# Kernel optimization log

Measured on AMD Instinct MI355X. Metric: run time of the kernel, lower is better.

## Reference

```python
import jax, jax.numpy as jnp
import numpy as np

N_RES = 131072
MSA_C = 384
HID = 128
N_BLOCK = 2
N_RESTYPE = 21


def l2_normalize(x, eps=1e-12):
    s = jnp.sum(x.astype(jnp.float32) ** 2, axis=-1, keepdims=True)
    return (x / jnp.sqrt(jnp.maximum(s, eps))).astype(x.dtype)


def quat_to_rot(q):
    q = q / jnp.sqrt(jnp.maximum(jnp.sum(q * q, axis=-1, keepdims=True), 1e-12))
    w, x, y, z = q[..., 0], q[..., 1], q[..., 2], q[..., 3]
    r00 = 1 - 2 * (y * y + z * z); r01 = 2 * (x * y - w * z); r02 = 2 * (x * z + w * y)
    r10 = 2 * (x * y + w * z); r11 = 1 - 2 * (x * x + z * z); r12 = 2 * (y * z - w * x)
    r20 = 2 * (x * z - w * y); r21 = 2 * (y * z + w * x); r22 = 1 - 2 * (x * x + y * y)
    return jnp.stack([jnp.stack([r00, r01, r02], -1),
                      jnp.stack([r10, r11, r12], -1),
                      jnp.stack([r20, r21, r22], -1)], axis=-2)


def setup_inputs() -> dict:
    key = jax.random.key(0)
    ks = jax.random.split(key, 20)
    d = {}
    d['affine'] = jax.random.normal(ks[0], (N_RES, 7), jnp.float32)
    d['rep0'] = jax.random.normal(ks[1], (N_RES, MSA_C), jnp.float32)
    d['rep1'] = jax.random.normal(ks[2], (N_RES, MSA_C), jnp.float32)
    d['aatype'] = jax.random.randint(ks[3], (N_RES,), 0, N_RESTYPE, jnp.int32)
    sc = 0.05
    d['w_in0'] = jax.random.normal(ks[4], (MSA_C, HID), jnp.float32) * sc
    d['b_in0'] = jnp.zeros((HID,), jnp.float32)
    d['w_in1'] = jax.random.normal(ks[5], (MSA_C, HID), jnp.float32) * sc
    d['b_in1'] = jnp.zeros((HID,), jnp.float32)
    d['Wr1'] = jax.random.normal(ks[6], (N_BLOCK, HID, HID), jnp.float32) * sc
    d['br1'] = jnp.zeros((N_BLOCK, HID), jnp.float32)
    d['Wr2'] = jax.random.normal(ks[7], (N_BLOCK, HID, HID), jnp.float32) * sc
    d['br2'] = jnp.zeros((N_BLOCK, HID), jnp.float32)
    d['w_ang'] = jax.random.normal(ks[8], (HID, 14), jnp.float32) * sc
    d['b_ang'] = jnp.zeros((14,), jnp.float32)
    # literature geometry tables (AF2 shapes; random stand-ins for correctness baseline)
    d['default_frames'] = jax.random.normal(ks[9], (N_RESTYPE, 8, 4, 4), jnp.float32)
    d['group_idx'] = jax.random.randint(ks[10], (N_RESTYPE, 14), 0, 8, jnp.int32)
    d['atom_mask'] = (jax.random.uniform(ks[11], (N_RESTYPE, 14)) > 0.2).astype(jnp.float32)
    d['lit_positions'] = jax.random.normal(ks[12], (N_RESTYPE, 14, 3), jnp.float32)
    return d


def reference(affine, rep0, rep1, aatype, w_in0, b_in0, w_in1, b_in1, Wr1, br1,
              Wr2, br2, w_ang, b_ang, default_frames, group_idx, atom_mask, lit_positions):
    # MLP trunk
    act = (jax.nn.relu(rep0) @ w_in0 + b_in0) + (jax.nn.relu(rep1) @ w_in1 + b_in1)
    for i in range(Wr1.shape[0]):
        old = act
        act = jax.nn.relu(act) @ Wr1[i] + br1[i]
        act = jax.nn.relu(act) @ Wr2[i] + br2[i]
        act = act + old
    n = act.shape[0]
    unnorm = (jax.nn.relu(act) @ w_ang + b_ang).reshape(n, 7, 2)
    angles = l2_normalize(unnorm)

    # backbone rigid from quat-affine
    rot_b = quat_to_rot(affine[:, :4])          # [N,3,3]
    trans_b = affine[:, 4:]                     # [N,3]

    # torsion_angles_to_frames
    sin = jnp.concatenate([jnp.zeros((n, 1), angles.dtype), angles[..., 0]], axis=-1)  # [N,8]
    cos = jnp.concatenate([jnp.ones((n, 1), angles.dtype), angles[..., 1]], axis=-1)
    z = jnp.zeros_like(sin); o = jnp.ones_like(sin)
    all_rots = jnp.stack([jnp.stack([o, z, z], -1),
                          jnp.stack([z, cos, -sin], -1),
                          jnp.stack([z, sin, cos], -1)], axis=-2)     # [N,8,3,3]
    m = default_frames[aatype]                   # [N,8,4,4] gather
    rot_f = jnp.einsum('ngij,ngjk->ngik', m[..., :3, :3], all_rots)   # [N,8,3,3]
    trans_f = m[..., :3, 3]                      # [N,8,3]

    def compose(r1, t1, r2, t2):
        return jnp.einsum('nij,njk->nik', r1, r2), jnp.einsum('nij,nj->ni', r1, t2) + t1

    r5, t5 = compose(rot_f[:, 4], trans_f[:, 4], rot_f[:, 5], trans_f[:, 5])  # chi2->backb
    r6, t6 = compose(r5, t5, rot_f[:, 6], trans_f[:, 6])                       # chi3->backb
    r7, t7 = compose(r6, t6, rot_f[:, 7], trans_f[:, 7])                       # chi4->backb
    rot_all = jnp.concatenate([rot_f[:, :5], jnp.stack([r5, r6, r7], 1)], axis=1)    # [N,8,3,3]
    trans_all = jnp.concatenate([trans_f[:, :5], jnp.stack([t5, t6, t7], 1)], axis=1)

    rot_g = jnp.einsum('nij,ngjk->ngik', rot_b, rot_all)                # [N,8,3,3]
    trans_g = jnp.einsum('nij,ngj->ngi', rot_b, trans_all) + trans_b[:, None]

    # frames_and_literature_positions_to_atom14_pos
    gm = jax.nn.one_hot(group_idx[aatype], 8, dtype=rot_g.dtype)        # [N,14,8]
    rot_a = jnp.einsum('nag,ngij->naij', gm, rot_g)                     # [N,14,3,3]
    trans_a = jnp.einsum('nag,ngi->nai', gm, trans_g)                   # [N,14,3]
    lit = lit_positions[aatype]                                         # [N,14,3]
    pos = jnp.einsum('naij,naj->nai', rot_a, lit) + trans_a
    pos = pos * atom_mask[aatype][..., None]
    return angles, unnorm, pos, rot_g, trans_g
```

## Files before the change

### kernel.cpp

```cpp
#include <hip/hip_runtime.h>
#include <stdint.h>

typedef _Float16 f16x8 __attribute__((ext_vector_type(8)));
typedef float floatx4 __attribute__((ext_vector_type(4)));

__device__ __forceinline__ void f2h2(float x, unsigned short& hi, unsigned short& lo) {
  _Float16 h = (_Float16)x;
  float r = (x - (float)h) * 2048.0f;
  _Float16 l = (_Float16)r;
  union { _Float16 f; unsigned short u; } a, b;
  a.f = h; b.f = l;
  hi = a.u; lo = b.u;
}

__device__ __forceinline__ void async_copy16(void* lds, const void* gsrc) {
  __builtin_amdgcn_global_load_lds(
      (const __attribute__((address_space(1))) unsigned int*)gsrc,
      (__attribute__((address_space(3))) unsigned int*)lds, 16, 0, 0);
}

__global__ __launch_bounds__(256) void k0_convert(
    const float* __restrict__ w_in0, const float* __restrict__ w_in1,
    const float* __restrict__ Wr1, const float* __restrict__ Wr2,
    const float* __restrict__ w_ang,
    unsigned short* __restrict__ btH, unsigned short* __restrict__ btL,
    unsigned short* __restrict__ wrtH, unsigned short* __restrict__ wrtL,
    unsigned short* __restrict__ angtH, unsigned short* __restrict__ angtL) {
  int e = blockIdx.x * 256 + threadIdx.x;
  if (e < 24 * 4096) {
    int s = e >> 12, rem = e & 4095;
    int ct = rem >> 9, lane = (rem >> 3) & 63, el = rem & 7;
    int n = ct * 16 + (lane & 15);
    int k = s * 32 + ((lane >> 4) << 3) + el;
    float v = (k < 384) ? w_in0[k * 128 + n] : w_in1[(k - 384) * 128 + n];
    f2h2(v, btH[e], btL[e]);
  }
  if (e < 4 * 128 * 128) {
    int mi = e / 16384, rem = e % 16384;
    int n = rem / 128, k = rem % 128;
    int blk = mi >> 1, which = mi & 1;
    const float* W = which ? Wr2 : Wr1;
    f2h2(W[blk * 16384 + k * 128 + n], wrtH[e], wrtL[e]);
  }
  if (e < 16 * 128) {
    int n = e / 128, k = e % 128;
    float v = (n < 14) ? w_ang[k * 14 + n] : 0.0f;
    f2h2(v, angtH[e], angtL[e]);
  }
}

__global__ __launch_bounds__(256) void k1_gemm_in(
    const float* __restrict__ rep0, const float* __restrict__ rep1,
    const float* __restrict__ b_in0, const float* __restrict__ b_in1,
    const unsigned short* __restrict__ btH, const unsigned short* __restrict__ btL,
    float* __restrict__ act) {
  __shared__ float Ab[2][4096];
  __shared__ unsigned short BH[2][4096];
  __shared__ unsigned short BL[2][4096];
  const int tid = threadIdx.x;
  const int lane = tid & 63, w = tid >> 6;
  const int m = lane & 15;
  const int row0 = blockIdx.x * 128;

  int aoff[4], adst[4];
#pragma unroll
  for (int r = 0; r < 4; ++r) {
    int rp = r & 1, h = r >> 1;
    aoff[r] = (row0 + (w * 2 + rp) * 16 + m) * 384 + ((lane >> 4) << 3) + h * 4;
    adst[r] = h * 2048 + (w * 2 + rp) * 256;
  }
  const int bsrc0 = (w * 2) * 512 + lane * 8;

  floatx4 acc1[2][8], acc2[2][8];
#pragma unroll
  for (int rt = 0; rt < 2; ++rt)
#pragma unroll
    for (int ct = 0; ct < 8; ++ct) {
      acc1[rt][ct] = (floatx4){0.f, 0.f, 0.f, 0.f};
      acc2[rt][ct] = (floatx4){0.f, 0.f, 0.f, 0.f};
    }

  auto stage = [&](int pb, int s) {
    const float* __restrict__ rep = (s < 12) ? rep0 : rep1;
    const int cb = (s < 12 ? s : s - 12) * 32;
#pragma unroll
    for (int r = 0; r < 4; ++r)
      async_copy16(&Ab[pb][adst[r]], rep + aoff[r] + cb);
#pragma unroll
    for (int r = 0; r < 2; ++r) {
      async_copy16(&BH[pb][(w * 2 + r) * 512], btH + (size_t)s * 4096 + bsrc0 + r * 512);
      async_copy16(&BL[pb][(w * 2 + r) * 512], btL + (size_t)s * 4096 + bsrc0 + r * 512);
    }
  };

  stage(0, 0);
#pragma unroll 2
  for (int s = 0; s < 24; ++s) {
    const int pb = s & 1;
    if (s < 23) {
      stage(pb ^ 1, s + 1);
      asm volatile("s_waitcnt vmcnt(8)" ::: "memory");
    } else {
      asm volatile("s_waitcnt vmcnt(0)" ::: "memory");
    }
    __builtin_amdgcn_s_barrier();
    asm volatile("" ::: "memory");

    f16x8 ah[2], al[2];
#pragma unroll
    for (int rt = 0; rt < 2; ++rt) {
      const float* ap = &Ab[pb][((w * 2 + rt) * 64 + lane) * 4];
      float4 x0 = *reinterpret_cast<const float4*>(ap);
      float4 x1 = *reinterpret_cast<const float4*>(ap + 2048);
      float xs[8] = {x0.x, x0.y, x0.z, x0.w, x1.x, x1.y, x1.z, x1.w};
#pragma unroll
      for (int e = 0; e < 8; ++e) {
        float x = fmaxf(xs[e], 0.f);
        _Float16 hh = (_Float16)x;
        ah[rt][e] = hh;
        al[rt][e] = (_Float16)((x - (float)hh) * 2048.0f);
      }
    }
#pragma unroll
    for (int ct = 0; ct < 8; ++ct) {
      f16x8 bh = *reinterpret_cast<const f16x8*>(&BH[pb][(ct * 64 + lane) * 8]);
      f16x8 bl = *reinterpret_cast<const f16x8*>(&BL[pb][(ct * 64 + lane) * 8]);
#pragma unroll
      for (int rt = 0; rt < 2; ++rt) {
        acc1[rt][ct] = __builtin_amdgcn_mfma_f32_16x16x32_f16(ah[rt], bh, acc1[rt][ct], 0, 0, 0);
        acc2[rt][ct] = __builtin_amdgcn_mfma_f32_16x16x32_f16(ah[rt], bl, acc2[rt][ct], 0, 0, 0);
        acc2[rt][ct] = __builtin_amdgcn_mfma_f32_16x16x32_f16(al[rt], bh, acc2[rt][ct], 0, 0, 0);
      }
    }
    asm volatile("" ::: "memory");
    __builtin_amdgcn_s_barrier();
    asm volatile("" ::: "memory");
  }

  const float S = 1.0f / 2048.0f;
  float* aout = act + ((size_t)blockIdx.x * 4 + w) * 4096 + (size_t)lane * 4;
#pragma unroll
  for (int rt = 0; rt < 2; ++rt)
#pragma unroll
    for (int ct = 0; ct < 8; ++ct) {
      int col = ct * 16 + m;
      float bias = b_in0[col] + b_in1[col];
      floatx4 v;
#pragma unroll
      for (int reg = 0; reg < 4; ++reg)
        v[reg] = acc1[rt][ct][reg] + acc2[rt][ct][reg] * S + bias;
      *reinterpret_cast<floatx4*>(aout + (rt * 8 + ct) * 256) = v;
    }
}

__global__ __launch_bounds__(256) void k2_resnet(
    const float* __restrict__ act,
    const unsigned short* __restrict__ wrtH, const unsigned short* __restrict__ wrtL,
    const float* __restrict__ br1, const float* __restrict__ br2,
    const unsigned short* __restrict__ angtH, const unsigned short* __restrict__ angtL,
    const float* __restrict__ b_ang, float* __restrict__ out_unnorm) {
  __shared__ unsigned short XbH[128 * 136], XbL[128 * 136];
  __shared__ unsigned short WbH[128 * 40], WbL[128 * 40];
  const int tid = threadIdx.x;
  const int lane = tid & 63, w = tid >> 6;
  const int q = lane >> 4, m = lane & 15;
  const int row0 = blockIdx.x * 128;
  const float S = 1.0f / 2048.0f;

  floatx4 cur[2][8];
  const float* ain = act + ((size_t)blockIdx.x * 4 + w) * 4096 + (size_t)lane * 4;
#pragma unroll
  for (int rt = 0; rt < 2; ++rt)
#pragma unroll
    for (int ct = 0; ct < 8; ++ct) {
      floatx4 v = *reinterpret_cast<const floatx4*>(ain + (rt * 8 + ct) * 256);
      cur[rt][ct] = v;
      int col = ct * 16 + m;
#pragma unroll
      for (int reg = 0; reg < 4; ++reg) {
        int rl = w * 32 + rt * 16 + q * 4 + reg;
        f2h2(fmaxf(v[reg], 0.f), XbH[rl * 136 + col], XbL[rl * 136 + col]);
      }
    }

  auto gemm = [&](const unsigned short* __restrict__ WH,
                  const unsigned short* __restrict__ WL,
                  floatx4 a1[2][8], floatx4 a2[2][8]) {
    for (int s = 0; s < 4; ++s) {
      __syncthreads();
#pragma unroll
      for (int r = 0; r < 2; ++r) {
        int c = tid + 256 * r;
        int nr = c >> 2, k8 = (c & 3) << 3;
        *reinterpret_cast<uint4*>(&WbH[nr * 40 + k8]) =
            *reinterpret_cast<const uint4*>(WH + nr * 128 + s * 32 + k8);
        *reinterpret_cast<uint4*>(&WbL[nr * 40 + k8]) =
            *reinterpret_cast<const uint4*>(WL + nr * 128 + s * 32 + k8);
      }
      __syncthreads();
      f16x8 ah[2], al[2];
#pragma unroll
      for (int rt = 0; rt < 2; ++rt) {
        ah[rt] = *reinterpret_cast<const f16x8*>(&XbH[(w * 32 + rt * 16 + m) * 136 + s * 32 + q * 8]);
        al[rt] = *reinterpret_cast<const f16x8*>(&XbL[(w * 32 + rt * 16 + m) * 136 + s * 32 + q * 8]);
      }
#pragma unroll
      for (int ct = 0; ct < 8; ++ct) {
        f16x8 bh = *reinterpret_cast<const f16x8*>(&WbH[(ct * 16 + m) * 40 + q * 8]);
        f16x8 bl = *reinterpret_cast<const f16x8*>(&WbL[(ct * 16 + m) * 40 + q * 8]);
#pragma unroll
        for (int rt = 0; rt < 2; ++rt) {
          a1[rt][ct] = __builtin_amdgcn_mfma_f32_16x16x32_f16(ah[rt], bh, a1[rt][ct], 0, 0, 0);
          a2[rt][ct] = __builtin_amdgcn_mfma_f32_16x16x32_f16(ah[rt], bl, a2[rt][ct], 0, 0, 0);
          a2[rt][ct] = __builtin_amdgcn_mfma_f32_16x16x32_f16(al[rt], bh, a2[rt][ct], 0, 0, 0);
        }
      }
    }
  };

  for (int i = 0; i < 2; ++i) {
    floatx4 a1[2][8], a2[2][8];
#pragma unroll
    for (int rt = 0; rt < 2; ++rt)
#pragma unroll
      for (int ct = 0; ct < 8; ++ct) {
        a1[rt][ct] = (floatx4){0.f, 0.f, 0.f, 0.f};
        a2[rt][ct] = (floatx4){0.f, 0.f, 0.f, 0.f};
      }
    gemm(wrtH + (size_t)(i * 2 + 0) * 16384, wrtL + (size_t)(i * 2 + 0) * 16384, a1, a2);
    __syncthreads();
#pragma unroll
    for (int rt = 0; rt < 2; ++rt)
#pragma unroll
      for (int ct = 0; ct < 8; ++ct) {
        int col = ct * 16 + m;
        float b = br1[i * 128 + col];
#pragma unroll
        for (int reg = 0; reg < 4; ++reg) {
          int rl = w * 32 + rt * 16 + q * 4 + reg;
          float v = a1[rt][ct][reg] + a2[rt][ct][reg] * S + b;
          f2h2(fmaxf(v, 0.f), XbH[rl * 136 + col], XbL[rl * 136 + col]);
        }
      }
    floatx4 c1[2][8], c2[2][8];
#pragma unroll
    for (int rt = 0; rt < 2; ++rt)
#pragma unroll
      for (int ct = 0; ct < 8; ++ct) {
        c1[rt][ct] = cur[rt][ct];
        c2[rt][ct] = (floatx4){0.f, 0.f, 0.f, 0.f};
      }
    gemm(wrtH + (size_t)(i * 2 + 1) * 16384, wrtL + (size_t)(i * 2 + 1) * 16384, c1, c2);
    __syncthreads();
#pragma unroll
    for (int rt = 0; rt < 2; ++rt)
#pragma unroll
      for (int ct = 0; ct < 8; ++ct) {
        int col = ct * 16 + m;
        float b = br2[i * 128 + col];
#pragma unroll
        for (int reg = 0; reg < 4; ++reg) {
          int rl = w * 32 + rt * 16 + q * 4 + reg;
          float v = c1[rt][ct][reg] + c2[rt][ct][reg] * S + b;
          cur[rt][ct][reg] = v;
          f2h2(fmaxf(v, 0.f), XbH[rl * 136 + col], XbL[rl * 136 + col]);
        }
      }
  }

  floatx4 A1[2], A2[2];
  A1[0] = (floatx4){0.f, 0.f, 0.f, 0.f}; A1[1] = A1[0];
  A2[0] = A1[0]; A2[1] = A1[0];
  for (int s = 0; s < 4; ++s) {
    __syncthreads();
    if (tid < 64) {
      int nr = tid >> 2, k8 = (tid & 3) << 3;
      *reinterpret_cast<uint4*>(&WbH[nr * 40 + k8]) =
          *reinterpret_cast<const uint4*>(angtH + nr * 128 + s * 32 + k8);
      *reinterpret_cast<uint4*>(&WbL[nr * 40 + k8]) =
          *reinterpret_cast<const uint4*>(angtL + nr * 128 + s * 32 + k8);
    }
    __syncthreads();
    f16x8 bh = *reinterpret_cast<const f16x8*>(&WbH[m * 40 + q * 8]);
    f16x8 bl = *reinterpret_cast<const f16x8*>(&WbL[m * 40 + q * 8]);
#pragma unroll
    for (int rt = 0; rt < 2; ++rt) {
      f16x8 ah = *reinterpret_cast<const f16x8*>(&XbH[(w * 32 + rt * 16 + m) * 136 + s * 32 + q * 8]);
      f16x8 al = *reinterpret_cast<const f16x8*>(&XbL[(w * 32 + rt * 16 + m) * 136 + s * 32 + q * 8]);
      A1[rt] = __builtin_amdgcn_mfma_f32_16x16x32_f16(ah, bh, A1[rt], 0, 0, 0);
      A2[rt] = __builtin_amdgcn_mfma_f32_16x16x32_f16(ah, bl, A2[rt], 0, 0, 0);
      A2[rt] = __builtin_amdgcn_mfma_f32_16x16x32_f16(al, bh, A2[rt], 0, 0, 0);
    }
  }
  if (m < 14) {
    float bias = b_ang[m];
#pragma unroll
    for (int rt = 0; rt < 2; ++rt)
#pragma unroll
      for (int reg = 0; reg < 4; ++reg) {
        int row = row0 + w * 32 + rt * 16 + q * 4 + reg;
        out_unnorm[(size_t)row * 14 + m] = A1[rt][reg] + A2[rt][reg] * S + bias;
      }
  }
}

__global__ __launch_bounds__(64) void k3_geom(
    const float* __restrict__ affine, const int* __restrict__ aatype,
    const float* __restrict__ dframes, const int* __restrict__ gidx,
    const float* __restrict__ amask, const float* __restrict__ lpos,
    float* __restrict__ out, int n) {
  __shared__ float lds[96 * 64];
  const int tid = threadIdx.x;
  const int r = blockIdx.x * 64 + tid;
  const size_t OFF0 = 0;
  const size_t OFF1 = (size_t)n * 14;
  const size_t OFF2 = (size_t)n * 28;
  const size_t OFF3 = (size_t)n * 70;
  const size_t OFF4 = (size_t)n * 142;

  float ang[14];
  const float* un = out + OFF1 + (size_t)r * 14;
#pragma unroll
  for (int j = 0; j < 7; ++j) {
    float a = un[2 * j], b = un[2 * j + 1];
    float inv = 1.0f / sqrtf(fmaxf(a * a + b * b, 1e-12f));
    ang[2 * j] = a * inv;
    ang[2 * j + 1] = b * inv;
    out[OFF0 + (size_t)r * 14 + 2 * j] = ang[2 * j];
    out[OFF0 + (size_t)r * 14 + 2 * j + 1] = ang[2 * j + 1];
  }

  const float* af = affine + (size_t)r * 7;
  float qw = af[0], qx = af[1], qy = af[2], qz = af[3];
  float qi = 1.0f / sqrtf(fmaxf(qw * qw + qx * qx + qy * qy + qz * qz, 1e-12f));
  qw *= qi; qx *= qi; qy *= qi; qz *= qi;
  float rb[9];
  rb[0] = 1.f - 2.f * (qy * qy + qz * qz);
  rb[1] = 2.f * (qx * qy - qw * qz);
  rb[2] = 2.f * (qx * qz + qw * qy);
  rb[3] = 2.f * (qx * qy + qw * qz);
  rb[4] = 1.f - 2.f * (qx * qx + qz * qz);
  rb[5] = 2.f * (qy * qz - qw * qx);
  rb[6] = 2.f * (qx * qz - qw * qy);
  rb[7] = 2.f * (qy * qz + qw * qx);
  rb[8] = 1.f - 2.f * (qx * qx + qy * qy);
  float tb0 = af[4], tb1 = af[5], tb2 = af[6];

  int aat = aatype[r];
  const float* mb = dframes + (size_t)aat * 128;
  float sa[8], ca[8];
  sa[0] = 0.f; ca[0] = 1.f;
#pragma unroll
  for (int g = 1; g < 8; ++g) { sa[g] = ang[(g - 1) * 2]; ca[g] = ang[(g - 1) * 2 + 1]; }

  float chr[9], cht[3];
#pragma unroll
  for (int g = 0; g < 8; ++g) {
    const float* M = mb + g * 16;
    float c = ca[g], s = sa[g];
    float rf[9], tf[3];
#pragma unroll
    for (int i = 0; i < 3; ++i) {
      float m1 = M[i * 4 + 1], m2 = M[i * 4 + 2];
      rf[i * 3 + 0] = M[i * 4 + 0];
      rf[i * 3 + 1] = m1 * c + m2 * s;
      rf[i * 3 + 2] = m2 * c - m1 * s;
      tf[i] = M[i * 4 + 3];
    }
    float ra[9], ta[3];
    if (g < 5) {
#pragma unroll
      for (int e = 0; e < 9; ++e) ra[e] = rf[e];
      ta[0] = tf[0]; ta[1] = tf[1]; ta[2] = tf[2];
      if (g == 4) {
#pragma unroll
        for (int e = 0; e < 9; ++e) chr[e] = rf[e];
        cht[0] = tf[0]; cht[1] = tf[1]; cht[2] = tf[2];
      }
    } else {
      float nr[9], nt[3];
#pragma unroll
      for (int i = 0; i < 3; ++i) {
#pragma unroll
        for (int j = 0; j < 3; ++j)
          nr[i * 3 + j] = chr[i * 3 + 0] * rf[0 + j] + chr[i * 3 + 1] * rf[3 + j] +
                          chr[i * 3 + 2] * rf[6 + j];
        nt[i] = chr[i * 3 + 0] * tf[0] + chr[i * 3 + 1] * tf[1] +
                chr[i * 3 + 2] * tf[2] + cht[i];
      }
#pragma unroll
      for (int e = 0; e < 9; ++e) { chr[e] = nr[e]; ra[e] = nr[e]; }
      cht[0] = nt[0]; cht[1] = nt[1]; cht[2] = nt[2];
      ta[0] = nt[0]; ta[1] = nt[1]; ta[2] = nt[2];
    }
    float rg[9], tg[3];
#pragma unroll
    for (int i = 0; i < 3; ++i) {
#pragma unroll
      for (int j = 0; j < 3; ++j)
        rg[i * 3 + j] = rb[i * 3 + 0] * ra[0 + j] + rb[i * 3 + 1] * ra[3 + j] +
                        rb[i * 3 + 2] * ra[6 + j];
      tg[i] = rb[i * 3 + 0] * ta[0] + rb[i * 3 + 1] * ta[1] + rb[i * 3 + 2] * ta[2];
    }
    tg[0] += tb0; tg[1] += tb1; tg[2] += tb2;
#pragma unroll
    for (int e = 0; e < 9; ++e) {
      out[OFF3 + (size_t)r * 72 + g * 9 + e] = rg[e];
      lds[(g * 12 + e) * 64 + tid] = rg[e];
    }
#pragma unroll
    for (int i = 0; i < 3; ++i) {
      out[OFF4 + (size_t)r * 24 + g * 3 + i] = tg[i];
      lds[(g * 12 + 9 + i) * 64 + tid] = tg[i];
    }
  }

#pragma unroll
  for (int a = 0; a < 14; ++a) {
    int gi = gidx[aat * 14 + a];
    float mask = amask[aat * 14 + a];
    const float* lp = lpos + (size_t)(aat * 14 + a) * 3;
    float l0 = lp[0], l1 = lp[1], l2 = lp[2];
    int b = gi * 12;
#pragma unroll
    for (int i = 0; i < 3; ++i) {
      float p = lds[(b + i * 3 + 0) * 64 + tid] * l0 +
                lds[(b + i * 3 + 1) * 64 + tid] * l1 +
                lds[(b + i * 3 + 2) * 64 + tid] * l2 + lds[(b + 9 + i) * 64 + tid];
      out[OFF2 + (size_t)r * 42 + a * 3 + i] = p * mask;
    }
  }
}

extern "C" void kernel_launch(void* const* d_in, const int* in_sizes, int n_in,
                              void* d_out, int out_size, void* d_ws, size_t ws_size,
                              hipStream_t stream) {
  const float* affine = (const float*)d_in[0];
  const float* rep0 = (const float*)d_in[1];
  const float* rep1 = (const float*)d_in[2];
  const int* aatype = (const int*)d_in[3];
  const float* w_in0 = (const float*)d_in[4];
  const float* b_in0 = (const float*)d_in[5];
  const float* w_in1 = (const float*)d_in[6];
  const float* b_in1 = (const float*)d_in[7];
  const float* Wr1 = (const float*)d_in[8];
  const float* br1 = (const float*)d_in[9];
  const float* Wr2 = (const float*)d_in[10];
  const float* br2 = (const float*)d_in[11];
  const float* w_ang = (const float*)d_in[12];
  const float* b_ang = (const float*)d_in[13];
  const float* dframes = (const float*)d_in[14];
  const int* gidx = (const int*)d_in[15];
  const float* amask = (const float*)d_in[16];
  const float* lpos = (const float*)d_in[17];
  float* out = (float*)d_out;

  const int n = in_sizes[0] / 7;

  char* ws = (char*)d_ws;
  unsigned short* btH = (unsigned short*)ws;
  unsigned short* btL = btH + 98304;
  unsigned short* wrtH = btL + 98304;
  unsigned short* wrtL = wrtH + 65536;
  unsigned short* angtH = wrtL + 65536;
  unsigned short* angtL = angtH + 2048;
  size_t w_bytes = (size_t)(2 * (98304 + 65536 + 2048)) * sizeof(unsigned short);
  size_t act_off = (w_bytes + 255) & ~(size_t)255;
  float* act;
  if (ws_size >= act_off + (size_t)n * 128 * sizeof(float)) {
    act = (float*)(ws + act_off);
  } else {
    act = out + (size_t)n * 28;
  }

  k0_convert<<<384, 256, 0, stream>>>(w_in0, w_in1, Wr1, Wr2, w_ang,
                                      btH, btL, wrtH, wrtL, angtH, angtL);
  k1_gemm_in<<<n / 128, 256, 0, stream>>>(rep0, rep1, b_in0, b_in1, btH, btL, act);
  k2_resnet<<<n / 128, 256, 0, stream>>>(act, wrtH, wrtL, br1, br2, angtH, angtL,
                                         b_ang, out + (size_t)n * 14);
  k3_geom<<<n / 64, 64, 0, stream>>>(affine, aatype, dframes, gidx, amask, lpos,
                                     out, n);
}
```

Baseline: 676.3 us.

## Retile input GEMM to 32-row blocks and coalesce geometry kernel stores via LDS

The input projection GEMM now uses 32-row blocks, each wave owning two output column tiles. It streams A through swizzled LDS in 192-column chunks and reads B fragments straight from global memory into registers with one-step prefetch. This is meant to raise occupancy and cut LDS traffic and barriers. Separately, the geometry kernel stages unnormalized angles, frames and atom positions in padded LDS and writes every output with coalesced float4 stores instead of strided per-row scalar stores. The cost is extra LDS use, more syncs, and B reloads from cache per block.

```diff
diff --git a/kernel.cpp b/kernel.cpp
--- a/kernel.cpp
+++ b/kernel.cpp
@@ -49,107 +49,120 @@
   }
 }
 
-__global__ __launch_bounds__(256) void k1_gemm_in(
+__global__ __launch_bounds__(256, 3) void k1_gemm_in(
     const float* __restrict__ rep0, const float* __restrict__ rep1,
     const float* __restrict__ b_in0, const float* __restrict__ b_in1,
     const unsigned short* __restrict__ btH, const unsigned short* __restrict__ btL,
     float* __restrict__ act) {
-  __shared__ float Ab[2][4096];
-  __shared__ unsigned short BH[2][4096];
-  __shared__ unsigned short BL[2][4096];
+  __shared__ float A[2][6144];
   const int tid = threadIdx.x;
   const int lane = tid & 63, w = tid >> 6;
-  const int m = lane & 15;
-  const int row0 = blockIdx.x * 128;
-
-  int aoff[4], adst[4];
-#pragma unroll
-  for (int r = 0; r < 4; ++r) {
-    int rp = r & 1, h = r >> 1;
-    aoff[r] = (row0 + (w * 2 + rp) * 16 + m) * 384 + ((lane >> 4) << 3) + h * 4;
-    adst[r] = h * 2048 + (w * 2 + rp) * 256;
-  }
-  const int bsrc0 = (w * 2) * 512 + lane * 8;
-
-  floatx4 acc1[2][8], acc2[2][8];
+  const int q = lane >> 4, m = lane & 15;
+  const int row0 = blockIdx.x * 32;
+
+  int srcf[6], dstb[6];
+#pragma unroll
+  for (int i = 0; i < 6; ++i) {
+    int sb = (w * 6 + i) * 1024 + lane * 16;
+    int row = sb / 768;
+    int colb = sb - row * 768;
+    int cswz = colb ^ ((row & 7) << 4);
+    srcf[i] = row * 384 + (cswz >> 2);
+    dstb[i] = (w * 6 + i) * 1024;
+  }
+
+  floatx4 acc1[2][2], acc2[2][2];
 #pragma unroll
   for (int rt = 0; rt < 2; ++rt)
 #pragma unroll
-    for (int ct = 0; ct < 8; ++ct) {
-      acc1[rt][ct] = (floatx4){0.f, 0.f, 0.f, 0.f};
-      acc2[rt][ct] = (floatx4){0.f, 0.f, 0.f, 0.f};
-    }
-
-  auto stage = [&](int pb, int s) {
-    const float* __restrict__ rep = (s < 12) ? rep0 : rep1;
-    const int cb = (s < 12 ? s : s - 12) * 32;
-#pragma unroll
-    for (int r = 0; r < 4; ++r)
-      async_copy16(&Ab[pb][adst[r]], rep + aoff[r] + cb);
-#pragma unroll
-    for (int r = 0; r < 2; ++r) {
-      async_copy16(&BH[pb][(w * 2 + r) * 512], btH + (size_t)s * 4096 + bsrc0 + r * 512);
-      async_copy16(&BL[pb][(w * 2 + r) * 512], btL + (size_t)s * 4096 + bsrc0 + r * 512);
-    }
+    for (int j = 0; j < 2; ++j) {
+      acc1[rt][j] = (floatx4){0.f, 0.f, 0.f, 0.f};
+      acc2[rt][j] = (floatx4){0.f, 0.f, 0.f, 0.f};
+    }
+
+  auto stage = [&](int buf, int p) {
+    const float* __restrict__ rp = (p < 2) ? rep0 : rep1;
+    const float* src = rp + (size_t)row0 * 384 + (p & 1) * 192;
+    char* db = (char*)&A[buf][0];
+#pragma unroll
+    for (int i = 0; i < 6; ++i) async_copy16(db + dstb[i], src + srcf[i]);
   };
 
+  auto loadB = [&](int sg, f16x8* bh, f16x8* bl) {
+#pragma unroll
+    for (int j = 0; j < 2; ++j) {
+      int ct = 2 * w + j;
+      size_t off = ((size_t)(sg * 8 + ct) * 64 + lane) * 8;
+      bh[j] = *reinterpret_cast<const f16x8*>(btH + off);
+      bl[j] = *reinterpret_cast<const f16x8*>(btL + off);
+    }
+  };
+
+  f16x8 bhc[2], blc[2];
+  loadB(0, bhc, blc);
   stage(0, 0);
-#pragma unroll 2
-  for (int s = 0; s < 24; ++s) {
-    const int pb = s & 1;
-    if (s < 23) {
-      stage(pb ^ 1, s + 1);
-      asm volatile("s_waitcnt vmcnt(8)" ::: "memory");
-    } else {
+
+  for (int p = 0; p < 4; ++p) {
+    __builtin_amdgcn_s_barrier();
+    if (p < 3) stage((p + 1) & 1, p + 1);
+    asm volatile("" ::: "memory");
+    if (p < 3)
+      asm volatile("s_waitcnt vmcnt(6)" ::: "memory");
+    else
       asm volatile("s_waitcnt vmcnt(0)" ::: "memory");
-    }
     __builtin_amdgcn_s_barrier();
     asm volatile("" ::: "memory");
 
-    f16x8 ah[2], al[2];
-#pragma unroll
-    for (int rt = 0; rt < 2; ++rt) {
-      const float* ap = &Ab[pb][((w * 2 + rt) * 64 + lane) * 4];
-      float4 x0 = *reinterpret_cast<const float4*>(ap);
-      float4 x1 = *reinterpret_cast<const float4*>(ap + 2048);
-      float xs[8] = {x0.x, x0.y, x0.z, x0.w, x1.x, x1.y, x1.z, x1.w};
-#pragma unroll
-      for (int e = 0; e < 8; ++e) {
-        float x = fmaxf(xs[e], 0.f);
-        _Float16 hh = (_Float16)x;
-        ah[rt][e] = hh;
-        al[rt][e] = (_Float16)((x - (float)hh) * 2048.0f);
-      }
-    }
-#pragma unroll
-    for (int ct = 0; ct < 8; ++ct) {
-      f16x8 bh = *reinterpret_cast<const f16x8*>(&BH[pb][(ct * 64 + lane) * 8]);
-      f16x8 bl = *reinterpret_cast<const f16x8*>(&BL[pb][(ct * 64 + lane) * 8]);
+    const float* Ab = &A[p & 1][0];
+#pragma unroll
+    for (int sl = 0; sl < 6; ++sl) {
+      int sg = p * 6 + sl;
+      f16x8 bhn[2], bln[2];
+      loadB(sg < 23 ? sg + 1 : 23, bhn, bln);
+
+      f16x8 ah[2], al[2];
 #pragma unroll
       for (int rt = 0; rt < 2; ++rt) {
-        acc1[rt][ct] = __builtin_amdgcn_mfma_f32_16x16x32_f16(ah[rt], bh, acc1[rt][ct], 0, 0, 0);
-        acc2[rt][ct] = __builtin_amdgcn_mfma_f32_16x16x32_f16(ah[rt], bl, acc2[rt][ct], 0, 0, 0);
-        acc2[rt][ct] = __builtin_amdgcn_mfma_f32_16x16x32_f16(al[rt], bh, acc2[rt][ct], 0, 0, 0);
-      }
-    }
-    asm volatile("" ::: "memory");
-    __builtin_amdgcn_s_barrier();
-    asm volatile("" ::: "memory");
+        int row = rt * 16 + m;
+        int boff = (row * 768 + sl * 128 + q * 32) ^ ((row & 7) << 4);
+        float4 x0 = *reinterpret_cast<const float4*>((const char*)Ab + boff);
+        float4 x1 = *reinterpret_cast<const float4*>((const char*)Ab + (boff ^ 16));
+        float xs[8] = {x0.x, x0.y, x0.z, x0.w, x1.x, x1.y, x1.z, x1.w};
+#pragma unroll
+        for (int e = 0; e < 8; ++e) {
+          float x = fmaxf(xs[e], 0.f);
+          _Float16 hh = (_Float16)x;
+          ah[rt][e] = hh;
+          al[rt][e] = (_Float16)((x - (float)hh) * 2048.0f);
+        }
+      }
+#pragma unroll
+      for (int j = 0; j < 2; ++j)
+#pragma unroll
+        for (int rt = 0; rt < 2; ++rt) {
+          acc1[rt][j] = __builtin_amdgcn_mfma_f32_16x16x32_f16(ah[rt], bhc[j], acc1[rt][j], 0, 0, 0);
+          acc2[rt][j] = __builtin_amdgcn_mfma_f32_16x16x32_f16(ah[rt], blc[j], acc2[rt][j], 0, 0, 0);
+          acc2[rt][j] = __builtin_amdgcn_mfma_f32_16x16x32_f16(al[rt], bhc[j], acc2[rt][j], 0, 0, 0);
+        }
+      bhc[0] = bhn[0]; bhc[1] = bhn[1];
+      blc[0] = bln[0]; blc[1] = bln[1];
+    }
   }
 
   const float S = 1.0f / 2048.0f;
-  float* aout = act + ((size_t)blockIdx.x * 4 + w) * 4096 + (size_t)lane * 4;
 #pragma unroll
   for (int rt = 0; rt < 2; ++rt)
 #pragma unroll
-    for (int ct = 0; ct < 8; ++ct) {
+    for (int j = 0; j < 2; ++j) {
+      int ct = 2 * w + j;
       int col = ct * 16 + m;
       float bias = b_in0[col] + b_in1[col];
       floatx4 v;
 #pragma unroll
       for (int reg = 0; reg < 4; ++reg)
-        v[reg] = acc1[rt][ct][reg] + acc2[rt][ct][reg] * S + bias;
-      *reinterpret_cast<floatx4*>(aout + (rt * 8 + ct) * 256) = v;
+        v[reg] = acc1[rt][j][reg] + acc2[rt][j][reg] * S + bias;
+      *reinterpret_cast<floatx4*>(
+          act + (((size_t)blockIdx.x * 2 + rt) * 8 + ct) * 256 + lane * 4) = v;
     }
 }
 
@@ -309,26 +322,46 @@
     const float* __restrict__ dframes, const int* __restrict__ gidx,
     const float* __restrict__ amask, const float* __restrict__ lpos,
     float* __restrict__ out, int n) {
-  __shared__ float lds[96 * 64];
+  __shared__ float lds[152 * 65];
   const int tid = threadIdx.x;
-  const int r = blockIdx.x * 64 + tid;
+  const int rblk = blockIdx.x * 64;
+  const int r = rblk + tid;
   const size_t OFF0 = 0;
   const size_t OFF1 = (size_t)n * 14;
   const size_t OFF2 = (size_t)n * 28;
   const size_t OFF3 = (size_t)n * 70;
   const size_t OFF4 = (size_t)n * 142;
 
+  {
+    const float* unb = out + OFF1 + (size_t)rblk * 14;
+#pragma unroll
+    for (int it = 0; it < 4; ++it) {
+      int f4 = it * 64 + tid;
+      if (f4 < 224) {
+        float4 v = *reinterpret_cast<const float4*>(unb + f4 * 4);
+#pragma unroll
+        for (int jj = 0; jj < 4; ++jj) {
+          int j = f4 * 4 + jj;
+          int rl = j / 14, c = j - rl * 14;
+          lds[(138 + c) * 65 + rl] = ((const float*)&v)[jj];
+        }
+      }
+    }
+  }
+  __syncthreads();
+
   float ang[14];
-  const float* un = out + OFF1 + (size_t)r * 14;
 #pragma unroll
   for (int j = 0; j < 7; ++j) {
-    float a = un[2 * j], b = un[2 * j + 1];
+    float a = lds[(138 + 2 * j) * 65 + tid];
+    float b = lds[(138 + 2 * j + 1) * 65 + tid];
     float inv = 1.0f / sqrtf(fmaxf(a * a + b * b, 1e-12f));
     ang[2 * j] = a * inv;
     ang[2 * j + 1] = b * inv;
-    out[OFF0 + (size_t)r * 14 + 2 * j] = ang[2 * j];
-    out[OFF0 + (size_t)r * 14 + 2 * j + 1] = ang[2 * j + 1];
-  }
+  }
+  __syncthreads();
+#pragma unroll
+  for (int j = 0; j < 14; ++j) lds[(138 + j) * 65 + tid] = ang[j];
 
   const float* af = affine + (size_t)r * 7;
   float qw = af[0], qx = af[1], qy = af[2], qz = af[3];
@@ -404,15 +437,9 @@
     }
     tg[0] += tb0; tg[1] += tb1; tg[2] += tb2;
 #pragma unroll
-    for (int e = 0; e < 9; ++e) {
-      out[OFF3 + (size_t)r * 72 + g * 9 + e] = rg[e];
-      lds[(g * 12 + e) * 64 + tid] = rg[e];
-    }
-#pragma unroll
-    for (int i = 0; i < 3; ++i) {
-      out[OFF4 + (size_t)r * 24 + g * 3 + i] = tg[i];
-      lds[(g * 12 + 9 + i) * 64 + tid] = tg[i];
-    }
+    for (int e = 0; e < 9; ++e) lds[(g * 12 + e) * 65 + tid] = rg[e];
+#pragma unroll
+    for (int i = 0; i < 3; ++i) lds[(g * 12 + 9 + i) * 65 + tid] = tg[i];
   }
 
 #pragma unroll
@@ -424,10 +451,80 @@
     int b = gi * 12;
 #pragma unroll
     for (int i = 0; i < 3; ++i) {
-      float p = lds[(b + i * 3 + 0) * 64 + tid] * l0 +
-                lds[(b + i * 3 + 1) * 64 + tid] * l1 +
-                lds[(b + i * 3 + 2) * 64 + tid] * l2 + lds[(b + 9 + i) * 64 + tid];
-      out[OFF2 + (size_t)r * 42 + a * 3 + i] = p * mask;
+      float p = lds[(b + i * 3 + 0) * 65 + tid] * l0 +
+                lds[(b + i * 3 + 1) * 65 + tid] * l1 +
+                lds[(b + i * 3 + 2) * 65 + tid] * l2 + lds[(b + 9 + i) * 65 + tid];
+      lds[(96 + a * 3 + i) * 65 + tid] = p * mask;
+    }
+  }
+  __syncthreads();
+
+  {
+    float* dst = out + OFF0 + (size_t)rblk * 14;
+#pragma unroll
+    for (int it = 0; it < 4; ++it) {
+      int f4 = it * 64 + tid;
+      if (f4 < 224) {
+        float4 v;
+#pragma unroll
+        for (int jj = 0; jj < 4; ++jj) {
+          int j = f4 * 4 + jj;
+          int rl = j / 14, c = j - rl * 14;
+          ((float*)&v)[jj] = lds[(138 + c) * 65 + rl];
+        }
+        *reinterpret_cast<float4*>(dst + f4 * 4) = v;
+      }
+    }
+  }
+  {
+    float* dst = out + OFF2 + (size_t)rblk * 42;
+#pragma unroll
+    for (int it = 0; it < 11; ++it) {
+      int f4 = it * 64 + tid;
+      if (f4 < 672) {
+        float4 v;
+#pragma unroll
+        for (int jj = 0; jj < 4; ++jj) {
+          int j = f4 * 4 + jj;
+          int rl = j / 42, c = j - rl * 42;
+          ((float*)&v)[jj] = lds[(96 + c) * 65 + rl];
+        }
+        *reinterpret_cast<float4*>(dst + f4 * 4) = v;
+      }
+    }
+  }
+  {
+    float* dst = out + OFF3 + (size_t)rblk * 72;
+#pragma unroll
+    for (int it = 0; it < 18; ++it) {
+      int f4 = it * 64 + tid;
+      int rl = f4 / 18;
+      int c4 = (f4 - rl * 18) * 4;
+      float4 v;
+#pragma unroll
+      for (int jj = 0; jj < 4; ++jj) {
+        int j = c4 + jj;
+        int g = j / 9, e = j - g * 9;
+        ((float*)&v)[jj] = lds[(g * 12 + e) * 65 + rl];
+      }
+      *reinterpret_cast<float4*>(dst + f4 * 4) = v;
+    }
+  }
+  {
+    float* dst = out + OFF4 + (size_t)rblk * 24;
+#pragma unroll
+    for (int it = 0; it < 6; ++it) {
+      int f4 = it * 64 + tid;
+      int rl = f4 / 6;
+      int c4 = (f4 - rl * 6) * 4;
+      float4 v;
+#pragma unroll
+      for (int jj = 0; jj < 4; ++jj) {
+        int j = c4 + jj;
+        int g = j / 3, i = j - g * 3;
+        ((float*)&v)[jj] = lds[(g * 12 + 9 + i) * 65 + rl];
+      }
+      *reinterpret_cast<float4*>(dst + f4 * 4) = v;
     }
   }
 }
@@ -475,7 +572,7 @@
 
   k0_convert<<<384, 256, 0, stream>>>(w_in0, w_in1, Wr1, Wr2, w_ang,
                                       btH, btL, wrtH, wrtL, angtH, angtL);
-  k1_gemm_in<<<n / 128, 256, 0, stream>>>(rep0, rep1, b_in0, b_in1, btH, btL, act);
+  k1_gemm_in<<<n / 32, 256, 0, stream>>>(rep0, rep1, b_in0, b_in1, btH, btL, act);
   k2_resnet<<<n / 128, 256, 0, stream>>>(act, wrtH, wrtL, br1, br2, angtH, angtL,
                                          b_ang, out + (size_t)n * 14);
   k3_geom<<<n / 64, 64, 0, stream>>>(affine, aatype, dframes, gidx, amask, lpos,
```

Result: faster. 626.7 us (-7.3%).
